# Kernel optimization log

Measured on AMD Instinct MI355X. Metric: run time of the kernel, lower is better.

## Reference

```python
import jax, jax.numpy as jnp
import numpy as np

POOL = 7
IMG_H, IMG_W = 1024, 1024
EPS = 1e-3  # keras BatchNormalization default epsilon


def crop_and_resize(fmap, boxes, ph, pw):
    # TF tf.image.crop_and_resize (bilinear), box_indices == batch index of each roi.
    # fmap: [B,H,W,C], boxes: [B,N,4] normalized (y1,x1,y2,x2) -> [B,N,ph,pw,C]
    B, H, W, C = fmap.shape
    y1, x1, y2, x2 = jnp.split(boxes, 4, axis=-1)  # each [B,N,1]
    fy = jnp.arange(ph, dtype=boxes.dtype) / (ph - 1)
    fx = jnp.arange(pw, dtype=boxes.dtype) / (pw - 1)
    ys = (y1 + (y2 - y1) * fy) * (H - 1)  # [B,N,ph]
    xs = (x1 + (x2 - x1) * fx) * (W - 1)  # [B,N,pw]
    y0 = jnp.floor(ys)
    x0 = jnp.floor(xs)
    wy = (ys - y0)[:, :, :, None, None]  # [B,N,ph,1,1]
    wx = (xs - x0)[:, :, None, :, None]  # [B,N,1,pw,1]
    y0i = jnp.clip(y0.astype(jnp.int32), 0, H - 1)
    y1i = jnp.clip(y0i + 1, 0, H - 1)
    x0i = jnp.clip(x0.astype(jnp.int32), 0, W - 1)
    x1i = jnp.clip(x0i + 1, 0, W - 1)
    b = jnp.arange(B)[:, None, None, None]
    yi0 = y0i[:, :, :, None]; yi1 = y1i[:, :, :, None]   # [B,N,ph,1]
    xi0 = x0i[:, :, None, :]; xi1 = x1i[:, :, None, :]   # [B,N,1,pw]
    v00 = fmap[b, yi0, xi0]  # [B,N,ph,pw,C]
    v01 = fmap[b, yi0, xi1]
    v10 = fmap[b, yi1, xi0]
    v11 = fmap[b, yi1, xi1]
    top = v00 + (v01 - v00) * wx
    bot = v10 + (v11 - v10) * wx
    return top + (bot - top) * wy


def pyramid_roi_align(rois, fmaps, pool):
    # rois are stop-gradient in the original layer
    rois = jax.lax.stop_gradient(rois)
    y1, x1, y2, x2 = jnp.split(rois, 4, axis=-1)
    h = y2 - y1
    w = x2 - x1
    scale = 256.0 / np.sqrt(float(IMG_H * IMG_W))
    lvl = jnp.log2(jnp.maximum(jnp.sqrt(h * w), 1e-9) / scale)
    lvl = jnp.clip(4 + jnp.round(lvl).astype(jnp.int32), 2, 5)[..., 0]  # [B,N]
    B, N = rois.shape[:2]
    C = fmaps[0].shape[-1]
    out = jnp.zeros((B, N, pool, pool, C), fmaps[0].dtype)
    for i, fm in enumerate(fmaps):  # levels 2..5, fixed small loop
        sel = (lvl == i + 2)[:, :, None, None, None]
        out = jnp.where(sel, crop_and_resize(fm, rois, pool, pool), out)
    return out


def bn_train(x, gamma, beta):
    # keras BatchNorm with training=True: biased batch stats over all axes but channel
    m = x.mean(axis=(0, 1))
    v = x.var(axis=(0, 1))
    return (x - m) * jax.lax.rsqrt(v + EPS) * gamma + beta


def setup_inputs() -> dict:
    key = jax.random.key(0)
    ks = jax.random.split(key, 12)
    B, N, C, F = 2, 1000, 256, 1024
    # rois: valid boxes, sizes spanning all pyramid levels
    tl = jax.random.uniform(ks[0], (B, N, 2), jnp.float32, 0.0, 0.6)
    sz = jax.random.uniform(ks[1], (B, N, 2), jnp.float32, 0.02, 0.4)
    br = jnp.minimum(tl + sz, 1.0)
    rois = jnp.concatenate([tl[..., :1], tl[..., 1:], br[..., :1], br[..., 1:]], axis=-1)
    s = 0.02
    return {
        "rois": rois,
        "p2": jax.random.normal(ks[2], (B, 256, 256, C), jnp.float32),
        "p3": jax.random.normal(ks[3], (B, 128, 128, C), jnp.float32),
        "p4": jax.random.normal(ks[4], (B, 64, 64, C), jnp.float32),
        "p5": jax.random.normal(ks[5], (B, 32, 32, C), jnp.float32),
        "conv1_w": jax.random.normal(ks[6], (POOL, POOL, C, F), jnp.float32) * s,
        "conv1_b": jnp.zeros((F,), jnp.float32),
        "bn1_g": jnp.ones((F,), jnp.float32),
        "bn1_b": jnp.zeros((F,), jnp.float32),
        "conv2_w": jax.random.normal(ks[7], (F, F), jnp.float32) * s,
        "conv2_b": jnp.zeros((F,), jnp.float32),
        "bn2_g": jnp.ones((F,), jnp.float32),
        "bn2_b": jnp.zeros((F,), jnp.float32),
        "cls_w": jax.random.normal(ks[8], (F, 2), jnp.float32) * s,
        "cls_b": jnp.zeros((2,), jnp.float32),
        "delta_w": jax.random.normal(ks[9], (F, 8), jnp.float32) * s,
        "delta_b": jnp.zeros((8,), jnp.float32),
    }


def reference(rois, p2, p3, p4, p5, conv1_w, conv1_b, bn1_g, bn1_b,
              conv2_w, conv2_b, bn2_g, bn2_b, cls_w, cls_b, delta_w, delta_b):
    B, N = rois.shape[:2]
    n_classes = cls_w.shape[-1]
    pooled = pyramid_roi_align(rois, (p2, p3, p4, p5), POOL)  # [B,N,7,7,C]
    # Conv2D(F,(7,7),'valid') on a 7x7 input == full contraction over (h,w,c)
    x = jnp.einsum('bnhwc,hwcf->bnf', pooled, conv1_w) + conv1_b
    x = jax.nn.relu(bn_train(x, bn1_g, bn1_b))
    x = x @ conv2_w + conv2_b  # 1x1 conv == dense
    shared = jax.nn.relu(bn_train(x, bn2_g, bn2_b))  # [B,N,F]
    logits = shared @ cls_w + cls_b                  # [B,N,n_classes]
    probs = jax.nn.softmax(logits, axis=-1)
    deltas = (shared @ delta_w + delta_b).reshape(B, N, n_classes, 4)
    return logits, probs, deltas
```

## Files before the change

kernel.cpp:

```cpp
#include <hip/hip_runtime.h>
#include <hip/hip_bf16.h>

#define NB     2
#define NROI   1000
#define CIN    256
#define FDIM   1024
#define M_ROWS 2000
#define K1     12544
#define EPSBN  1e-3f
#define MN     (M_ROWS * FDIM)

typedef short bf16x8 __attribute__((ext_vector_type(8)));
typedef short bf16x4 __attribute__((ext_vector_type(4)));
typedef float f32x4  __attribute__((ext_vector_type(4)));

__device__ __forceinline__ void gld_lds16(const void* g, void* l) {
  __builtin_amdgcn_global_load_lds((const __attribute__((address_space(1))) char*)g,
                                   (__attribute__((address_space(3))) char*)l, 16, 0, 0);
}

__global__ __launch_bounds__(256) void prep_kernel(
    const float* __restrict__ rois,
    const float* __restrict__ p2, const float* __restrict__ p3,
    const float* __restrict__ p4, const float* __restrict__ p5,
    __hip_bfloat16* __restrict__ pooled,
    const float* __restrict__ conv1_w, __hip_bfloat16* __restrict__ w1t,
    const float* __restrict__ conv2_w, __hip_bfloat16* __restrict__ w2t,
    float* __restrict__ stats) {
  __shared__ float tt[64][65];
  int idx = blockIdx.x;
  int t = threadIdx.x;

  if (idx == 0) {
#pragma unroll
    for (int i = 0; i < 4; i++)
      ((f32x4*)stats)[t + i * 256] = f32x4{0, 0, 0, 0};
    return;
  }

  if (idx < 1 + M_ROWS) {
    int rn = idx - 1;
    int b = rn / NROI;

    const float* roi = rois + (size_t)rn * 4;
    float y1 = roi[0], x1 = roi[1], y2 = roi[2], x2 = roi[3];
    float h = y2 - y1, w = x2 - x1;
    float lvl = log2f(fmaxf(sqrtf(h * w), 1e-9f) * 4.0f);
    int li = 4 + (int)rintf(lvl);
    li = min(max(li, 2), 5) - 2;

    const float* fm; int H;
    switch (li) {
      case 0:  fm = p2; H = 256; break;
      case 1:  fm = p3; H = 128; break;
      case 2:  fm = p4; H = 64;  break;
      default: fm = p5; H = 32;  break;
    }
    int W = H;
    const float* fb = fm + (size_t)b * H * W * CIN;

    int lane = t & 63, wv = t >> 6;
    int c4 = lane * 4;

    for (int pos = wv; pos < 49; pos += 4) {
      int py = pos / 7, px = pos - py * 7;
      float fy = (float)py / 6.0f, fx = (float)px / 6.0f;
      float ys = (y1 + (y2 - y1) * fy) * (float)(H - 1);
      float xs = (x1 + (x2 - x1) * fx) * (float)(W - 1);
      float y0f = floorf(ys), x0f = floorf(xs);
      float wy = ys - y0f, wx = xs - x0f;
      int y0 = min(max((int)y0f, 0), H - 1);
      int x0 = min(max((int)x0f, 0), W - 1);
      int y1i = min(y0 + 1, H - 1);
      int x1i = min(x0 + 1, W - 1);

      f32x4 v00 = *(const f32x4*)(fb + ((size_t)y0 * W + x0) * CIN + c4);
      f32x4 v01 = *(const f32x4*)(fb + ((size_t)y0 * W + x1i) * CIN + c4);
      f32x4 v10 = *(const f32x4*)(fb + ((size_t)y1i * W + x0) * CIN + c4);
      f32x4 v11 = *(const f32x4*)(fb + ((size_t)y1i * W + x1i) * CIN + c4);

      f32x4 top = v00 + (v01 - v00) * wx;
      f32x4 bot = v10 + (v11 - v10) * wx;
      f32x4 val = top + (bot - top) * wy;

      bf16x4 o;
#pragma unroll
      for (int j = 0; j < 4; j++) {
        __hip_bfloat16 hh = __float2bfloat16(val[j]);
        o[j] = *reinterpret_cast<short*>(&hh);
      }
      *(bf16x4*)((short*)pooled + ((size_t)rn * 49 + pos) * CIN + c4) = o;
    }
    return;
  }

  const float* W; short* WT; int K, N, bx, by;
  if (idx < 1 + M_ROWS + 3136) {
    int wk = idx - (1 + M_ROWS);
    W = conv1_w; WT = (short*)w1t; K = K1; N = FDIM;
    bx = wk % 196; by = wk / 196;
  } else {
    int wk = idx - (1 + M_ROWS + 3136);
    W = conv2_w; WT = (short*)w2t; K = FDIM; N = FDIM;
    bx = wk % 16; by = wk / 16;
  }
  int k0 = bx * 64, n0 = by * 64;
  int r = t >> 2, c = t & 3;
#pragma unroll
  for (int i = 0; i < 4; i++) {
    int cg = c * 4 + i;
    f32x4 v = *(const f32x4*)(W + (size_t)(k0 + r) * N + n0 + cg * 4);
#pragma unroll
    for (int j = 0; j < 4; j++) tt[cg * 4 + j][r] = v[j];
  }
  __syncthreads();
  int n = t >> 2, g = t & 3;
#pragma unroll
  for (int i = 0; i < 2; i++) {
    int seg = g * 2 + i;
    bf16x8 o;
#pragma unroll
    for (int j = 0; j < 8; j++) {
      __hip_bfloat16 hh = __float2bfloat16(tt[n][seg * 8 + j]);
      o[j] = *reinterpret_cast<short*>(&hh);
    }
    *(bf16x8*)(WT + (size_t)(n0 + n) * K + k0 + seg * 8) = o;
  }
}

template<int KSLICES>
__global__ __launch_bounds__(512) void gemm8w(const short* __restrict__ A,
                                              const short* __restrict__ BT,
                                              float* __restrict__ P,
                                              int M, int N, int K) {
  __shared__ short As[4 * 128 * 32];
  __shared__ short Bs[4 * 256 * 32];

  int nwg = gridDim.x;
  int bid = blockIdx.x;
  int cpx = nwg >> 3;
  int wg = (bid & 7) * cpx + (bid >> 3);

  int MT = (M + 127) >> 7;
  int NTn = N >> 8;
  int tiles = MT * NTn;
  int ks = wg / tiles;
  int rem = wg % tiles;
  int tm = rem % MT, tn = rem / MT;
  int m0 = tm * 128, n0 = tn * 256;
  int Kc = K / KSLICES;
  int NT = Kc >> 6;
  size_t kb = (size_t)ks * Kc;

  int tid = threadIdx.x;
  int lane = tid & 63, wid = tid >> 6;
  int wr = wid >> 2, wc = wid & 3;

  int srow = tid >> 2;
  int g = (tid & 3) ^ (srow & 3);
  const short* Agb  = A  + (size_t)min(m0 + srow, M - 1) * K + kb + g * 8;
  const short* Bgb0 = BT + (size_t)(n0 + srow) * K + kb + g * 8;
  const short* Bgb1 = Bgb0 + (size_t)128 * K;
  int aoff  = wid * 512;
  int boff0 = wid * 512;
  int boff1 = 4096 + wid * 512;

  int lr = lane & 15;
  int slotoff = ((lane >> 4) ^ (lane & 3)) * 8;
  const short* Ard = As + (wr * 64 + lr) * 32 + slotoff;
  const short* Brd = Bs + (wc * 64 + lr) * 32 + slotoff;

  f32x4 acc[4][4] = {};

#define STAGE(s) do {                                                        \
    int ts_ = (s) >> 1, kh_ = (s) & 1, b_ = ts_ & 1;                         \
    int ko_ = ts_ * 64 + kh_ * 32;                                           \
    short* Ad_ = (short*)As + (b_ * 2 + kh_) * 4096 + aoff;                  \
    short* Bd_ = (short*)Bs + (b_ * 2 + kh_) * 8192;                         \
    gld_lds16(Agb + ko_, Ad_);                                               \
    gld_lds16(Bgb0 + ko_, Bd_ + boff0);                                      \
    gld_lds16(Bgb1 + ko_, Bd_ + boff1);                                      \
  } while (0)

  STAGE(0); STAGE(1); STAGE(2);

  for (int t = 0; t < NT; ++t) {
    int b = t & 1;
#pragma unroll
    for (int kh = 0; kh < 2; ++kh) {
      __builtin_amdgcn_sched_barrier(0);
      if (t < NT - 1)      asm volatile("s_waitcnt vmcnt(6)" ::: "memory");
      else if (kh == 0)    asm volatile("s_waitcnt vmcnt(3)" ::: "memory");
      else                 asm volatile("s_waitcnt vmcnt(0)" ::: "memory");
      __builtin_amdgcn_s_barrier();
      __builtin_amdgcn_sched_barrier(0);

      const short* Ab = Ard + (b * 2 + kh) * 4096;
      const short* Bb = Brd + (b * 2 + kh) * 8192;
      bf16x8 af[4], bf_[4];
#pragma unroll
      for (int mi = 0; mi < 4; mi++) af[mi] = *(const bf16x8*)(Ab + mi * 512);
#pragma unroll
      for (int ni = 0; ni < 4; ni++) bf_[ni] = *(const bf16x8*)(Bb + ni * 512);

      if (kh == 0) { if (t + 1 < NT) STAGE(2 * t + 3); }
      else         { if (t + 2 < NT) STAGE(2 * t + 4); }

      __builtin_amdgcn_sched_barrier(0);
      asm volatile("s_waitcnt lgkmcnt(0)" ::: "memory");
      __builtin_amdgcn_sched_barrier(0);
      __builtin_amdgcn_s_setprio(1);
#pragma unroll
      for (int mi = 0; mi < 4; mi++)
#pragma unroll
        for (int ni = 0; ni < 4; ni++)
          acc[mi][ni] = __builtin_amdgcn_mfma_f32_16x16x32_bf16(af[mi], bf_[ni], acc[mi][ni], 0, 0, 0);
      __builtin_amdgcn_s_setprio(0);
    }
  }
#undef STAGE

  float* Pb = P + (size_t)ks * M * N;
  int crow = (lane >> 4) * 4, ccol = lane & 15;
#pragma unroll
  for (int mi = 0; mi < 4; mi++) {
    int rb = m0 + wr * 64 + mi * 16 + crow;
#pragma unroll
    for (int ni = 0; ni < 4; ni++) {
      int col = n0 + wc * 64 + ni * 16 + ccol;
#pragma unroll
      for (int r = 0; r < 4; r++) {
        int row = rb + r;
        if (row < M) Pb[(size_t)row * N + col] = acc[mi][ni][r];
      }
    }
  }
}

__global__ void reduce_bias_stats(const float* __restrict__ P, const float* __restrict__ bias,
                                  float* __restrict__ X, float* __restrict__ stats,
                                  int M, int KS) {
  int t = threadIdx.x;
  int col = t * 4;
  f32x4 bv = *(const f32x4*)(bias + col);
  f32x4 s = {0, 0, 0, 0}, q = {0, 0, 0, 0};
  for (int r = blockIdx.x; r < M; r += gridDim.x) {
    size_t base = (size_t)r * FDIM + col;
    f32x4 v = *(const f32x4*)(P + base);
    for (int c = 1; c < KS; c++)
      v = v + *(const f32x4*)(P + (size_t)c * MN + base);
    v = v + bv;
    *(f32x4*)(X + base) = v;
    s = s + v;
    q = q + v * v;
  }
#pragma unroll
  for (int j = 0; j < 4; j++) {
    atomicAdd(&stats[col + j], s[j]);
    atomicAdd(&stats[FDIM + col + j], q[j]);
  }
}

__global__ void bn_norm_relu_bf16(const float* __restrict__ X, const float* __restrict__ stats,
                                  const float* __restrict__ g, const float* __restrict__ bta,
                                  __hip_bfloat16* __restrict__ obf, int M) {
  int idx = blockIdx.x * blockDim.x + threadIdx.x;
  if (idx >= M * FDIM) return;
  int f = idx & (FDIM - 1);
  float inv_m = 1.0f / (float)M;
  float mean = stats[f] * inv_m;
  float var = stats[FDIM + f] * inv_m - mean * mean;
  float xn = (X[idx] - mean) * rsqrtf(var + EPSBN) * g[f] + bta[f];
  obf[idx] = __float2bfloat16(fmaxf(xn, 0.0f));
}

__global__ void heads_bn(const float* __restrict__ X2, const float* __restrict__ stats,
                         const float* __restrict__ gg, const float* __restrict__ bb,
                         const float* __restrict__ cls_w, const float* __restrict__ cls_b,
                         const float* __restrict__ dw, const float* __restrict__ db,
                         float* __restrict__ out) {
  int row = blockIdx.x * 4 + (threadIdx.x >> 6);
  int lane = threadIdx.x & 63;
  if (row >= M_ROWS) return;
  const float* xrow = X2 + (size_t)row * FDIM;
  float inv_m = 1.0f / (float)M_ROWS;
  float a[10];
#pragma unroll
  for (int j = 0; j < 10; j++) a[j] = 0.0f;
  for (int k = lane; k < FDIM; k += 64) {
    float mean = stats[k] * inv_m;
    float var = stats[FDIM + k] * inv_m - mean * mean;
    float v = fmaxf((xrow[k] - mean) * rsqrtf(var + EPSBN) * gg[k] + bb[k], 0.0f);
    a[0] += v * cls_w[k * 2 + 0];
    a[1] += v * cls_w[k * 2 + 1];
#pragma unroll
    for (int j = 0; j < 8; j++) a[2 + j] += v * dw[k * 8 + j];
  }
#pragma unroll
  for (int j = 0; j < 10; j++)
    for (int o = 32; o > 0; o >>= 1) a[j] += __shfl_xor(a[j], o, 64);
  if (lane == 0) {
    float l0 = a[0] + cls_b[0], l1 = a[1] + cls_b[1];
    out[row * 2 + 0] = l0;
    out[row * 2 + 1] = l1;
    float mx = fmaxf(l0, l1);
    float e0 = expf(l0 - mx), e1 = expf(l1 - mx);
    float inv = 1.0f / (e0 + e1);
    out[4000 + row * 2 + 0] = e0 * inv;
    out[4000 + row * 2 + 1] = e1 * inv;
#pragma unroll
    for (int j = 0; j < 8; j++) out[8000 + row * 8 + j] = a[2 + j] + db[j];
  }
}

extern "C" void kernel_launch(void* const* d_in, const int* in_sizes, int n_in,
                              void* d_out, int out_size, void* d_ws, size_t ws_size,
                              hipStream_t stream) {
  const float* rois    = (const float*)d_in[0];
  const float* p2      = (const float*)d_in[1];
  const float* p3      = (const float*)d_in[2];
  const float* p4      = (const float*)d_in[3];
  const float* p5      = (const float*)d_in[4];
  const float* conv1_w = (const float*)d_in[5];
  const float* conv1_b = (const float*)d_in[6];
  const float* bn1_g   = (const float*)d_in[7];
  const float* bn1_b   = (const float*)d_in[8];
  const float* conv2_w = (const float*)d_in[9];
  const float* conv2_b = (const float*)d_in[10];
  const float* bn2_g   = (const float*)d_in[11];
  const float* bn2_b   = (const float*)d_in[12];
  const float* cls_w   = (const float*)d_in[13];
  const float* cls_b   = (const float*)d_in[14];
  const float* delta_w = (const float*)d_in[15];
  const float* delta_b = (const float*)d_in[16];
  float* out = (float*)d_out;

  char* ws = (char*)d_ws;
  size_t off = 0;
  __hip_bfloat16* pooled = (__hip_bfloat16*)(ws + off); off += (size_t)M_ROWS * K1 * 2;
  __hip_bfloat16* w1t    = (__hip_bfloat16*)(ws + off); off += (size_t)K1 * FDIM * 2;
  __hip_bfloat16* w2t    = (__hip_bfloat16*)(ws + off); off += (size_t)FDIM * FDIM * 2;
  float* stats1          = (float*)(ws + off);          off += 2 * FDIM * 4;
  float* stats2          = (float*)(ws + off);          off += 2 * FDIM * 4;
  char*  Preg            = ws + off;                    off += (size_t)4 * MN * 4;
  float* part1        = (float*)Preg;
  float* x1           = (float*)Preg;
  __hip_bfloat16* x1n = (__hip_bfloat16*)pooled;
  float* part2        = (float*)Preg;
  float* x2           = (float*)Preg;

  prep_kernel<<<1 + M_ROWS + 3136 + 256, 256, 0, stream>>>(
      rois, p2, p3, p4, p5, pooled, conv1_w, w1t, conv2_w, w2t, stats1);

  gemm8w<4><<<256, 512, 0, stream>>>((const short*)pooled, (const short*)w1t, part1,
                                     M_ROWS, FDIM, K1);
  reduce_bias_stats<<<256, 256, 0, stream>>>(part1, conv1_b, x1, stats1, M_ROWS, 4);

  bn_norm_relu_bf16<<<MN / 256, 256, 0, stream>>>(x1, stats1, bn1_g, bn1_b, x1n, M_ROWS);

  gemm8w<4><<<256, 512, 0, stream>>>((const short*)x1n, (const short*)w2t, part2,
                                     M_ROWS, FDIM, FDIM);
  reduce_bias_stats<<<256, 256, 0, stream>>>(part2, conv2_b, x2, stats2, M_ROWS, 4);

  heads_bn<<<(M_ROWS + 3) / 4, 256, 0, stream>>>(x2, stats2, bn2_g, bn2_b,
                                                 cls_w, cls_b, delta_w, delta_b, out);

  (void)in_sizes; (void)n_in; (void)out_size; (void)ws_size;
}
```

Baseline: 210.8 us.

## Use 256x256-tile split-K GEMM for conv1, batch ROI loads, restructure heads kernel

Adds a gemm256 kernel for the first GEMM with 256x256 output tiles, a 4-slot global_load_lds pipeline and 7-way split-K across 224 workgroups, and enlarges the partial-sum workspace to match. The ROI-align loop now issues the bilinear loads for two pooled positions before blending either, to hide gather latency. heads_bn precomputes BN scale/shift and transposed head weights into shared memory and handles 16 rows per block. The larger tile raises data reuse and MFMA density but uses more registers and LDS and adds split-K reduction traffic.

```diff
diff --git a/kernel.cpp b/kernel.cpp
--- a/kernel.cpp
+++ b/kernel.cpp
@@ -62,27 +62,28 @@
     int lane = t & 63, wv = t >> 6;
     int c4 = lane * 4;
 
-    for (int pos = wv; pos < 49; pos += 4) {
+    auto coords = [&](int pos, const float*& q00, const float*& q01,
+                      const float*& q10, const float*& q11, float& wy, float& wx) {
       int py = pos / 7, px = pos - py * 7;
       float fy = (float)py / 6.0f, fx = (float)px / 6.0f;
       float ys = (y1 + (y2 - y1) * fy) * (float)(H - 1);
       float xs = (x1 + (x2 - x1) * fx) * (float)(W - 1);
       float y0f = floorf(ys), x0f = floorf(xs);
-      float wy = ys - y0f, wx = xs - x0f;
+      wy = ys - y0f; wx = xs - x0f;
       int y0 = min(max((int)y0f, 0), H - 1);
       int x0 = min(max((int)x0f, 0), W - 1);
       int y1i = min(y0 + 1, H - 1);
       int x1i = min(x0 + 1, W - 1);
-
-      f32x4 v00 = *(const f32x4*)(fb + ((size_t)y0 * W + x0) * CIN + c4);
-      f32x4 v01 = *(const f32x4*)(fb + ((size_t)y0 * W + x1i) * CIN + c4);
-      f32x4 v10 = *(const f32x4*)(fb + ((size_t)y1i * W + x0) * CIN + c4);
-      f32x4 v11 = *(const f32x4*)(fb + ((size_t)y1i * W + x1i) * CIN + c4);
-
+      q00 = fb + ((size_t)y0 * W + x0) * CIN + c4;
+      q01 = fb + ((size_t)y0 * W + x1i) * CIN + c4;
+      q10 = fb + ((size_t)y1i * W + x0) * CIN + c4;
+      q11 = fb + ((size_t)y1i * W + x1i) * CIN + c4;
+    };
+    auto emit = [&](int pos, f32x4 v00, f32x4 v01, f32x4 v10, f32x4 v11,
+                    float wy, float wx) {
       f32x4 top = v00 + (v01 - v00) * wx;
       f32x4 bot = v10 + (v11 - v10) * wx;
       f32x4 val = top + (bot - top) * wy;
-
       bf16x4 o;
 #pragma unroll
       for (int j = 0; j < 4; j++) {
@@ -90,6 +91,24 @@
         o[j] = *reinterpret_cast<short*>(&hh);
       }
       *(bf16x4*)((short*)pooled + ((size_t)rn * 49 + pos) * CIN + c4) = o;
+    };
+
+    for (int pos = wv; pos < 49; pos += 8) {
+      const float *a00, *a01, *a10, *a11; float awy, awx;
+      coords(pos, a00, a01, a10, a11, awy, awx);
+      f32x4 va00 = *(const f32x4*)a00, va01 = *(const f32x4*)a01;
+      f32x4 va10 = *(const f32x4*)a10, va11 = *(const f32x4*)a11;
+      int pos2 = pos + 4;
+      if (pos2 < 49) {
+        const float *b00, *b01, *b10, *b11; float bwy, bwx;
+        coords(pos2, b00, b01, b10, b11, bwy, bwx);
+        f32x4 vb00 = *(const f32x4*)b00, vb01 = *(const f32x4*)b01;
+        f32x4 vb10 = *(const f32x4*)b10, vb11 = *(const f32x4*)b11;
+        emit(pos, va00, va01, va10, va11, awy, awx);
+        emit(pos2, vb00, vb01, vb10, vb11, bwy, bwx);
+      } else {
+        emit(pos, va00, va01, va10, va11, awy, awx);
+      }
     }
     return;
   }
@@ -125,6 +144,113 @@
       o[j] = *reinterpret_cast<short*>(&hh);
     }
     *(bf16x8*)(WT + (size_t)(n0 + n) * K + k0 + seg * 8) = o;
+  }
+}
+
+template<int KSLICES>
+__global__ __launch_bounds__(512) void gemm256(const short* __restrict__ A,
+                                               const short* __restrict__ BT,
+                                               float* __restrict__ P,
+                                               int M, int N, int K) {
+  __shared__ short As[4 * 8192];
+  __shared__ short Bs[4 * 8192];
+
+  int nwg = gridDim.x;
+  int bid = blockIdx.x;
+  int cpx = nwg >> 3;
+  int wg = (bid & 7) * cpx + (bid >> 3);
+
+  int MT = (M + 255) >> 8;
+  int NTn = N >> 8;
+  int tiles = MT * NTn;
+  int ks = wg / tiles;
+  int rem = wg % tiles;
+  int tm = rem % MT, tn = rem / MT;
+  int m0 = tm * 256, n0 = tn * 256;
+  int Kc = K / KSLICES;
+  int S = Kc >> 5;
+  size_t kb = (size_t)ks * Kc;
+
+  int tid = threadIdx.x;
+  int lane = tid & 63, wid = tid >> 6;
+  int wr = wid >> 2, wc = wid & 3;
+
+  int row0 = tid >> 2, row1 = 128 + row0;
+  int g0 = (tid & 3) ^ (row0 & 3);
+  int g1 = (tid & 3) ^ (row1 & 3);
+  const short* Ag0 = A + (size_t)min(m0 + row0, M - 1) * K + kb + g0 * 8;
+  const short* Ag1 = A + (size_t)min(m0 + row1, M - 1) * K + kb + g1 * 8;
+  const short* Bg0 = BT + (size_t)(n0 + row0) * K + kb + g0 * 8;
+  const short* Bg1 = BT + (size_t)(n0 + row1) * K + kb + g1 * 8;
+  int wbase = wid * 512;
+
+  int lr = lane & 15;
+  int slotoff = ((lane >> 4) ^ (lane & 3)) * 8;
+  const short* Ard = As + (wr * 128 + lr) * 32 + slotoff;
+  const short* Brd = Bs + (wc * 64 + lr) * 32 + slotoff;
+
+  f32x4 acc[8][4] = {};
+
+#define STAGE(s) do {                                                         \
+    int ts_ = (s) >> 1, kh_ = (s) & 1;                                        \
+    int slot_ = ((ts_ & 1) << 1) | kh_;                                       \
+    int ko_ = ts_ * 64 + kh_ * 32;                                            \
+    short* Ad_ = (short*)As + slot_ * 8192;                                   \
+    short* Bd_ = (short*)Bs + slot_ * 8192;                                   \
+    gld_lds16(Ag0 + ko_, Ad_ + wbase);                                        \
+    gld_lds16(Ag1 + ko_, Ad_ + 4096 + wbase);                                 \
+    gld_lds16(Bg0 + ko_, Bd_ + wbase);                                        \
+    gld_lds16(Bg1 + ko_, Bd_ + 4096 + wbase);                                 \
+  } while (0)
+
+  STAGE(0); STAGE(1); STAGE(2);
+
+  for (int s = 0; s < S; ++s) {
+    int slot = (((s >> 1) & 1) << 1) | (s & 1);
+    __builtin_amdgcn_sched_barrier(0);
+    if (s < S - 2)       asm volatile("s_waitcnt vmcnt(8)" ::: "memory");
+    else if (s == S - 2) asm volatile("s_waitcnt vmcnt(4)" ::: "memory");
+    else                 asm volatile("s_waitcnt vmcnt(0)" ::: "memory");
+    __builtin_amdgcn_s_barrier();
+    __builtin_amdgcn_sched_barrier(0);
+
+    const short* Ab = Ard + slot * 8192;
+    const short* Bb = Brd + slot * 8192;
+    bf16x8 af[8], bf_[4];
+#pragma unroll
+    for (int mi = 0; mi < 8; mi++) af[mi] = *(const bf16x8*)(Ab + mi * 512);
+#pragma unroll
+    for (int ni = 0; ni < 4; ni++) bf_[ni] = *(const bf16x8*)(Bb + ni * 512);
+
+    if (s + 3 < S) STAGE(s + 3);
+
+    __builtin_amdgcn_sched_barrier(0);
+    asm volatile("s_waitcnt lgkmcnt(0)" ::: "memory");
+    __builtin_amdgcn_sched_barrier(0);
+    __builtin_amdgcn_s_setprio(1);
+#pragma unroll
+    for (int mi = 0; mi < 8; mi++)
+#pragma unroll
+      for (int ni = 0; ni < 4; ni++)
+        acc[mi][ni] = __builtin_amdgcn_mfma_f32_16x16x32_bf16(af[mi], bf_[ni], acc[mi][ni], 0, 0, 0);
+    __builtin_amdgcn_s_setprio(0);
+  }
+#undef STAGE
+
+  float* Pb = P + (size_t)ks * M * N;
+  int crow = (lane >> 4) * 4, ccol = lane & 15;
+#pragma unroll
+  for (int mi = 0; mi < 8; mi++) {
+    int rb = m0 + wr * 128 + mi * 16 + crow;
+#pragma unroll
+    for (int ni = 0; ni < 4; ni++) {
+      int col = n0 + wc * 64 + ni * 16 + ccol;
+#pragma unroll
+      for (int r = 0; r < 4; r++) {
+        int row = rb + r;
+        if (row < M) Pb[(size_t)row * N + col] = acc[mi][ni][r];
+      }
+    }
   }
 }
 
@@ -274,42 +400,60 @@
   obf[idx] = __float2bfloat16(fmaxf(xn, 0.0f));
 }
 
-__global__ void heads_bn(const float* __restrict__ X2, const float* __restrict__ stats,
-                         const float* __restrict__ gg, const float* __restrict__ bb,
-                         const float* __restrict__ cls_w, const float* __restrict__ cls_b,
-                         const float* __restrict__ dw, const float* __restrict__ db,
-                         float* __restrict__ out) {
-  int row = blockIdx.x * 4 + (threadIdx.x >> 6);
-  int lane = threadIdx.x & 63;
-  if (row >= M_ROWS) return;
-  const float* xrow = X2 + (size_t)row * FDIM;
+__global__ __launch_bounds__(256) void heads_bn(
+    const float* __restrict__ X2, const float* __restrict__ stats,
+    const float* __restrict__ gg, const float* __restrict__ bb,
+    const float* __restrict__ cls_w, const float* __restrict__ cls_b,
+    const float* __restrict__ dw, const float* __restrict__ db,
+    float* __restrict__ out) {
+  __shared__ float scale[FDIM], shift[FDIM];
+  __shared__ float clsT[2][FDIM];
+  __shared__ float dwT[8][FDIM];
+  int t = threadIdx.x;
   float inv_m = 1.0f / (float)M_ROWS;
-  float a[10];
-#pragma unroll
-  for (int j = 0; j < 10; j++) a[j] = 0.0f;
-  for (int k = lane; k < FDIM; k += 64) {
-    float mean = stats[k] * inv_m;
-    float var = stats[FDIM + k] * inv_m - mean * mean;
-    float v = fmaxf((xrow[k] - mean) * rsqrtf(var + EPSBN) * gg[k] + bb[k], 0.0f);
-    a[0] += v * cls_w[k * 2 + 0];
-    a[1] += v * cls_w[k * 2 + 1];
-#pragma unroll
-    for (int j = 0; j < 8; j++) a[2 + j] += v * dw[k * 8 + j];
-  }
-#pragma unroll
-  for (int j = 0; j < 10; j++)
-    for (int o = 32; o > 0; o >>= 1) a[j] += __shfl_xor(a[j], o, 64);
-  if (lane == 0) {
-    float l0 = a[0] + cls_b[0], l1 = a[1] + cls_b[1];
-    out[row * 2 + 0] = l0;
-    out[row * 2 + 1] = l1;
-    float mx = fmaxf(l0, l1);
-    float e0 = expf(l0 - mx), e1 = expf(l1 - mx);
-    float inv = 1.0f / (e0 + e1);
-    out[4000 + row * 2 + 0] = e0 * inv;
-    out[4000 + row * 2 + 1] = e1 * inv;
-#pragma unroll
-    for (int j = 0; j < 8; j++) out[8000 + row * 8 + j] = a[2 + j] + db[j];
+  for (int i = t; i < FDIM; i += 256) {
+    float m = stats[i] * inv_m;
+    float va = stats[FDIM + i] * inv_m - m * m;
+    float sc = rsqrtf(va + EPSBN) * gg[i];
+    scale[i] = sc;
+    shift[i] = bb[i] - m * sc;
+    clsT[0][i] = cls_w[i * 2];
+    clsT[1][i] = cls_w[i * 2 + 1];
+#pragma unroll
+    for (int j = 0; j < 8; j++) dwT[j][i] = dw[i * 8 + j];
+  }
+  __syncthreads();
+
+  int lane = t & 63, wv = t >> 6;
+#pragma unroll
+  for (int i = 0; i < 4; i++) {
+    int row = blockIdx.x * 16 + i * 4 + wv;
+    const float* xrow = X2 + (size_t)row * FDIM;
+    float a[10];
+#pragma unroll
+    for (int j = 0; j < 10; j++) a[j] = 0.0f;
+    for (int k = lane; k < FDIM; k += 64) {
+      float v = fmaxf(xrow[k] * scale[k] + shift[k], 0.0f);
+      a[0] += v * clsT[0][k];
+      a[1] += v * clsT[1][k];
+#pragma unroll
+      for (int j = 0; j < 8; j++) a[2 + j] += v * dwT[j][k];
+    }
+#pragma unroll
+    for (int j = 0; j < 10; j++)
+      for (int o = 32; o > 0; o >>= 1) a[j] += __shfl_xor(a[j], o, 64);
+    if (lane == 0) {
+      float l0 = a[0] + cls_b[0], l1 = a[1] + cls_b[1];
+      out[row * 2 + 0] = l0;
+      out[row * 2 + 1] = l1;
+      float mx = fmaxf(l0, l1);
+      float e0 = expf(l0 - mx), e1 = expf(l1 - mx);
+      float inv = 1.0f / (e0 + e1);
+      out[4000 + row * 2 + 0] = e0 * inv;
+      out[4000 + row * 2 + 1] = e1 * inv;
+#pragma unroll
+      for (int j = 0; j < 8; j++) out[8000 + row * 8 + j] = a[2 + j] + db[j];
+    }
   }
 }
 
@@ -342,7 +486,7 @@
   __hip_bfloat16* w2t    = (__hip_bfloat16*)(ws + off); off += (size_t)FDIM * FDIM * 2;
   float* stats1          = (float*)(ws + off);          off += 2 * FDIM * 4;
   float* stats2          = (float*)(ws + off);          off += 2 * FDIM * 4;
-  char*  Preg            = ws + off;                    off += (size_t)4 * MN * 4;
+  char*  Preg            = ws + off;                    off += (size_t)7 * MN * 4;
   float* part1        = (float*)Preg;
   float* x1           = (float*)Preg;
   __hip_bfloat16* x1n = (__hip_bfloat16*)pooled;
@@ -352,9 +496,9 @@
   prep_kernel<<<1 + M_ROWS + 3136 + 256, 256, 0, stream>>>(
       rois, p2, p3, p4, p5, pooled, conv1_w, w1t, conv2_w, w2t, stats1);
 
-  gemm8w<4><<<256, 512, 0, stream>>>((const short*)pooled, (const short*)w1t, part1,
-                                     M_ROWS, FDIM, K1);
-  reduce_bias_stats<<<256, 256, 0, stream>>>(part1, conv1_b, x1, stats1, M_ROWS, 4);
+  gemm256<7><<<224, 512, 0, stream>>>((const short*)pooled, (const short*)w1t, part1,
+                                      M_ROWS, FDIM, K1);
+  reduce_bias_stats<<<256, 256, 0, stream>>>(part1, conv1_b, x1, stats1, M_ROWS, 7);
 
   bn_norm_relu_bf16<<<MN / 256, 256, 0, stream>>>(x1, stats1, bn1_g, bn1_b, x1n, M_ROWS);
 
@@ -362,8 +506,8 @@
                                      M_ROWS, FDIM, FDIM);
   reduce_bias_stats<<<256, 256, 0, stream>>>(part2, conv2_b, x2, stats2, M_ROWS, 4);
 
-  heads_bn<<<(M_ROWS + 3) / 4, 256, 0, stream>>>(x2, stats2, bn2_g, bn2_b,
-                                                 cls_w, cls_b, delta_w, delta_b, out);
+  heads_bn<<<125, 256, 0, stream>>>(x2, stats2, bn2_g, bn2_b,
+                                    cls_w, cls_b, delta_w, delta_b, out);
 
   (void)in_sizes; (void)n_in; (void)out_size; (void)ws_size;
 }
```

New measurement: 228.2 us. 1.08x slower.

## Split ROI pooling across two blocks, remap GEMM tiles, cache BN params in heads

Applied to the files above, without the earlier changes.

ROI pooling now uses two blocks per ROI, each handling alternating groups of positions, which doubles the parallelism of that phase. The GEMM block-to-tile mapping is replaced with a fixed bit-twiddled layout that groups K-slices and M tiles differently, presumably to change XCD/L2 locality; it is hardcoded for 256 blocks and 16x4x4 tiles. The heads kernel precomputes BN scale/shift and transposed head weights in shared memory and processes 16 rows per block, cutting redundant per-row rsqrt and strided weight loads.

```diff
diff --git a/kernel.cpp b/kernel.cpp
--- a/kernel.cpp
+++ b/kernel.cpp
@@ -38,8 +38,9 @@
     return;
   }
 
-  if (idx < 1 + M_ROWS) {
-    int rn = idx - 1;
+  if (idx < 1 + 2 * M_ROWS) {
+    int rr = idx - 1;
+    int rn = rr >> 1, half = rr & 1;
     int b = rn / NROI;
 
     const float* roi = rois + (size_t)rn * 4;
@@ -62,7 +63,7 @@
     int lane = t & 63, wv = t >> 6;
     int c4 = lane * 4;
 
-    for (int pos = wv; pos < 49; pos += 4) {
+    for (int pos = half * 4 + wv; pos < 49; pos += 8) {
       int py = pos / 7, px = pos - py * 7;
       float fy = (float)py / 6.0f, fx = (float)px / 6.0f;
       float ys = (y1 + (y2 - y1) * fy) * (float)(H - 1);
@@ -95,12 +96,12 @@
   }
 
   const float* W; short* WT; int K, N, bx, by;
-  if (idx < 1 + M_ROWS + 3136) {
-    int wk = idx - (1 + M_ROWS);
+  if (idx < 1 + 2 * M_ROWS + 3136) {
+    int wk = idx - (1 + 2 * M_ROWS);
     W = conv1_w; WT = (short*)w1t; K = K1; N = FDIM;
     bx = wk % 196; by = wk / 196;
   } else {
-    int wk = idx - (1 + M_ROWS + 3136);
+    int wk = idx - (1 + 2 * M_ROWS + 3136);
     W = conv2_w; WT = (short*)w2t; K = FDIM; N = FDIM;
     bx = wk % 16; by = wk / 16;
   }
@@ -136,17 +137,10 @@
   __shared__ short As[4 * 128 * 32];
   __shared__ short Bs[4 * 256 * 32];
 
-  int nwg = gridDim.x;
   int bid = blockIdx.x;
-  int cpx = nwg >> 3;
-  int wg = (bid & 7) * cpx + (bid >> 3);
-
-  int MT = (M + 127) >> 7;
-  int NTn = N >> 8;
-  int tiles = MT * NTn;
-  int ks = wg / tiles;
-  int rem = wg % tiles;
-  int tm = rem % MT, tn = rem / MT;
+  int ks = (bid & 7) >> 1;
+  int tm = ((bid & 1) << 3) | (bid >> 5);
+  int tn = (bid >> 3) & 3;
   int m0 = tm * 128, n0 = tn * 256;
   int Kc = K / KSLICES;
   int NT = Kc >> 6;
@@ -274,42 +268,60 @@
   obf[idx] = __float2bfloat16(fmaxf(xn, 0.0f));
 }
 
-__global__ void heads_bn(const float* __restrict__ X2, const float* __restrict__ stats,
-                         const float* __restrict__ gg, const float* __restrict__ bb,
-                         const float* __restrict__ cls_w, const float* __restrict__ cls_b,
-                         const float* __restrict__ dw, const float* __restrict__ db,
-                         float* __restrict__ out) {
-  int row = blockIdx.x * 4 + (threadIdx.x >> 6);
-  int lane = threadIdx.x & 63;
-  if (row >= M_ROWS) return;
-  const float* xrow = X2 + (size_t)row * FDIM;
+__global__ __launch_bounds__(256) void heads_bn(
+    const float* __restrict__ X2, const float* __restrict__ stats,
+    const float* __restrict__ gg, const float* __restrict__ bb,
+    const float* __restrict__ cls_w, const float* __restrict__ cls_b,
+    const float* __restrict__ dw, const float* __restrict__ db,
+    float* __restrict__ out) {
+  __shared__ float scale[FDIM], shift[FDIM];
+  __shared__ float clsT[2][FDIM];
+  __shared__ float dwT[8][FDIM];
+  int t = threadIdx.x;
   float inv_m = 1.0f / (float)M_ROWS;
-  float a[10];
-#pragma unroll
-  for (int j = 0; j < 10; j++) a[j] = 0.0f;
-  for (int k = lane; k < FDIM; k += 64) {
-    float mean = stats[k] * inv_m;
-    float var = stats[FDIM + k] * inv_m - mean * mean;
-    float v = fmaxf((xrow[k] - mean) * rsqrtf(var + EPSBN) * gg[k] + bb[k], 0.0f);
-    a[0] += v * cls_w[k * 2 + 0];
-    a[1] += v * cls_w[k * 2 + 1];
-#pragma unroll
-    for (int j = 0; j < 8; j++) a[2 + j] += v * dw[k * 8 + j];
-  }
-#pragma unroll
-  for (int j = 0; j < 10; j++)
-    for (int o = 32; o > 0; o >>= 1) a[j] += __shfl_xor(a[j], o, 64);
-  if (lane == 0) {
-    float l0 = a[0] + cls_b[0], l1 = a[1] + cls_b[1];
-    out[row * 2 + 0] = l0;
-    out[row * 2 + 1] = l1;
-    float mx = fmaxf(l0, l1);
-    float e0 = expf(l0 - mx), e1 = expf(l1 - mx);
-    float inv = 1.0f / (e0 + e1);
-    out[4000 + row * 2 + 0] = e0 * inv;
-    out[4000 + row * 2 + 1] = e1 * inv;
-#pragma unroll
-    for (int j = 0; j < 8; j++) out[8000 + row * 8 + j] = a[2 + j] + db[j];
+  for (int i = t; i < FDIM; i += 256) {
+    float m = stats[i] * inv_m;
+    float va = stats[FDIM + i] * inv_m - m * m;
+    float sc = rsqrtf(va + EPSBN) * gg[i];
+    scale[i] = sc;
+    shift[i] = bb[i] - m * sc;
+    clsT[0][i] = cls_w[i * 2];
+    clsT[1][i] = cls_w[i * 2 + 1];
+#pragma unroll
+    for (int j = 0; j < 8; j++) dwT[j][i] = dw[i * 8 + j];
+  }
+  __syncthreads();
+
+  int lane = t & 63, wv = t >> 6;
+#pragma unroll
+  for (int i = 0; i < 4; i++) {
+    int row = blockIdx.x * 16 + i * 4 + wv;
+    const float* xrow = X2 + (size_t)row * FDIM;
+    float a[10];
+#pragma unroll
+    for (int j = 0; j < 10; j++) a[j] = 0.0f;
+    for (int k = lane; k < FDIM; k += 64) {
+      float v = fmaxf(xrow[k] * scale[k] + shift[k], 0.0f);
+      a[0] += v * clsT[0][k];
+      a[1] += v * clsT[1][k];
+#pragma unroll
+      for (int j = 0; j < 8; j++) a[2 + j] += v * dwT[j][k];
+    }
+#pragma unroll
+    for (int j = 0; j < 10; j++)
+      for (int o = 32; o > 0; o >>= 1) a[j] += __shfl_xor(a[j], o, 64);
+    if (lane == 0) {
+      float l0 = a[0] + cls_b[0], l1 = a[1] + cls_b[1];
+      out[row * 2 + 0] = l0;
+      out[row * 2 + 1] = l1;
+      float mx = fmaxf(l0, l1);
+      float e0 = expf(l0 - mx), e1 = expf(l1 - mx);
+      float inv = 1.0f / (e0 + e1);
+      out[4000 + row * 2 + 0] = e0 * inv;
+      out[4000 + row * 2 + 1] = e1 * inv;
+#pragma unroll
+      for (int j = 0; j < 8; j++) out[8000 + row * 8 + j] = a[2 + j] + db[j];
+    }
   }
 }
 
@@ -349,7 +361,7 @@
   float* part2        = (float*)Preg;
   float* x2           = (float*)Preg;
 
-  prep_kernel<<<1 + M_ROWS + 3136 + 256, 256, 0, stream>>>(
+  prep_kernel<<<1 + 2 * M_ROWS + 3136 + 256, 256, 0, stream>>>(
       rois, p2, p3, p4, p5, pooled, conv1_w, w1t, conv2_w, w2t, stats1);
 
   gemm8w<4><<<256, 512, 0, stream>>>((const short*)pooled, (const short*)w1t, part1,
@@ -362,8 +374,8 @@
                                      M_ROWS, FDIM, FDIM);
   reduce_bias_stats<<<256, 256, 0, stream>>>(part2, conv2_b, x2, stats2, M_ROWS, 4);
 
-  heads_bn<<<(M_ROWS + 3) / 4, 256, 0, stream>>>(x2, stats2, bn2_g, bn2_b,
-                                                 cls_w, cls_b, delta_w, delta_b, out);
+  heads_bn<<<125, 256, 0, stream>>>(x2, stats2, bn2_g, bn2_b,
+                                    cls_w, cls_b, delta_w, delta_b, out);
 
   (void)in_sizes; (void)n_in; (void)out_size; (void)ws_size;
 }
```

Result: slower. 226.3 us (+7.4%).
